# Kernel optimization log

Measured on AMD Instinct MI355X. Metric: run time of the kernel, lower is better.

Reference implementation:

```python
import jax, jax.numpy as jnp
import numpy as np

B, T, C, H = 2, 2048, 1024, 16
HS = C // H            # head_size = 64
HID = 2730             # 2*((2*(4*C)//3 + 1)//2) with multiple_of=2
EPS = 1e-6


def setup_inputs() -> dict:
    key = jax.random.key(0)
    ks = jax.random.split(key, 10)
    s = 0.02
    x = jax.random.normal(ks[0], (B, T, C), dtype=jnp.float32)
    Wq = jax.random.normal(ks[1], (H, HS, C), dtype=jnp.float32) * s
    Wk = jax.random.normal(ks[2], (H, HS, C), dtype=jnp.float32) * s
    Wv = jax.random.normal(ks[3], (H, HS, C), dtype=jnp.float32) * s
    Wo = jax.random.normal(ks[4], (C, C), dtype=jnp.float32) * s
    bo = jnp.zeros((C,), jnp.float32)
    w1 = jax.random.normal(ks[5], (HID, C), dtype=jnp.float32) * s
    b1 = jnp.zeros((HID,), jnp.float32)
    w2 = jax.random.normal(ks[6], (HID, C), dtype=jnp.float32) * s
    b2 = jnp.zeros((HID,), jnp.float32)
    w3 = jax.random.normal(ks[7], (C, HID), dtype=jnp.float32) * s
    b3 = jnp.zeros((C,), jnp.float32)
    ln1_w = jnp.ones((C,), jnp.float32)
    ln2_w = jnp.ones((C,), jnp.float32)
    # RoPE tables: freqs_cis = polar(1, outer(t, 1/theta^(2i/d)))
    inv = 1.0 / (10000.0 ** (jnp.arange(0, HS, 2, dtype=jnp.float32) / HS))  # [HS/2]
    ang = jnp.arange(T, dtype=jnp.float32)[:, None] * inv[None, :]           # [T, HS/2]
    return dict(x=x, ln1_w=ln1_w, Wq=Wq, Wk=Wk, Wv=Wv, Wo=Wo, bo=bo,
                w1=w1, b1=b1, w2=w2, b2=b2, w3=w3, b3=b3, ln2_w=ln2_w,
                cos=jnp.cos(ang), sin=jnp.sin(ang))


def _rmsnorm(x, w):
    return x / jnp.sqrt(jnp.mean(x * x, axis=-1, keepdims=True) + EPS) * w


def _rope(x, cos, sin):
    # x: [B,H,T,HS]; cos/sin: [T, HS/2] -> complex rotation on (even,odd) pairs
    xr = x.reshape(*x.shape[:-1], HS // 2, 2)
    x0, x1 = xr[..., 0], xr[..., 1]
    c = cos[None, None]; s = sin[None, None]
    o0 = x0 * c - x1 * s
    o1 = x0 * s + x1 * c
    return jnp.stack([o0, o1], axis=-1).reshape(x.shape)


def _swish_bug(x):
    # faithful to source: x * (1/1 + exp(-x)) == x * (1 + exp(-x))
    return x * (1.0 + jnp.exp(-x))


def reference(x, ln1_w, Wq, Wk, Wv, Wo, bo, w1, b1, w2, b2, w3, b3, ln2_w, cos, sin):
    # Block (norm='rms'): x = l1(x); x = x + attn(x); x = l2(x); x = x + ffn(x)
    x1 = _rmsnorm(x, ln1_w)
    # batched per-head projections (Linear has no bias in Head)
    q = jnp.einsum('btc,hdc->bhtd', x1, Wq)
    k = jnp.einsum('btc,hdc->bhtd', x1, Wk)
    v = jnp.einsum('btc,hdc->bhtd', x1, Wv)
    # source: xq,xk = apply_rotary_emb(key, query); query,key = xq,xk;
    # wei = key @ query^T == rot(query) @ rot(key)^T  -> standard attention
    q = _rope(q, cos, sin)
    k = _rope(k, cos, sin)
    scores = jnp.einsum('bhtd,bhsd->bhts', q, k) * (HS ** -0.5)
    mask = jnp.tril(jnp.ones((T, T), dtype=bool))
    scores = jnp.where(mask[None, None], scores, -jnp.inf)
    wei = jax.nn.softmax(scores, axis=-1)
    attn = jnp.einsum('bhts,bhsd->bhtd', wei, v)
    attn = attn.transpose(0, 2, 1, 3).reshape(B, T, C)  # concat heads
    attn = attn @ Wo.T + bo
    x2 = x1 + attn
    x3 = _rmsnorm(x2, ln2_w)
    h = _swish_bug(x3 @ w1.T + b1) * (x3 @ w2.T + b2)
    ffn = h @ w3.T + b3
    return x3 + ffn
```

## Files before the change

kernel.cpp:

```cpp
#include <hip/hip_runtime.h>
#include <hip/hip_bf16.h>

#define Bv 2
#define Tv 2048
#define Cv 1024
#define Hv 16
#define HSv 64
#define HIDv 2730
#define HIDP 2816
#define Mv 4096

using bf16x8 = __attribute__((ext_vector_type(8))) __bf16;
using f32x4  = __attribute__((ext_vector_type(4))) float;
typedef unsigned long long ull;

__device__ __forceinline__ void gload_lds16(const void* g, void* l) {
    auto gp = (const __attribute__((address_space(1))) unsigned int*)(unsigned long long)(uintptr_t)g;
    auto lp = (__attribute__((address_space(3))) unsigned int*)(unsigned int)(uintptr_t)l;
    __builtin_amdgcn_global_load_lds(gp, lp, 16, 0, 0);
}

struct CastSeg { const float* s; __bf16* d; long nsrc; long ntot; int sc; int dc; };
struct CastArgs { CastSeg seg[7]; };

__global__ __launch_bounds__(256) void k_castall(CastArgs a) {
    long gid = (long)blockIdx.x * 256 + threadIdx.x;
    long gstr = (long)gridDim.x * 256;
#pragma unroll 1
    for (int g = 0; g < 7; ++g) {
        CastSeg sg = a.seg[g];
        if (sg.sc == 0) {
            long n4 = sg.ntot >> 2;
            for (long i = gid; i < n4; i += gstr) {
                long base = i * 4;
                float4 v = {0.f, 0.f, 0.f, 0.f};
                if (base < sg.nsrc) v = *(const float4*)(sg.s + base);
                __bf16 o[4] = {(__bf16)v.x, (__bf16)v.y, (__bf16)v.z, (__bf16)v.w};
                *(ull*)(sg.d + base) = *(ull*)o;
            }
        } else {
            long n8 = sg.ntot >> 3;
            for (long i8 = gid; i8 < n8; i8 += gstr) {
                long base = i8 * 8;
                int r = (int)(base / sg.dc), c = (int)(base % sg.dc);
                __bf16 o[8];
                const float* srow = sg.s + (long)r * sg.sc + c;
                if (c + 8 <= sg.sc) {
#pragma unroll
                    for (int q = 0; q < 4; ++q) {
                        float2 v = *(const float2*)(srow + q * 2);
                        o[q * 2] = (__bf16)v.x; o[q * 2 + 1] = (__bf16)v.y;
                    }
                } else {
#pragma unroll
                    for (int e = 0; e < 8; ++e)
                        o[e] = (c + e < sg.sc) ? (__bf16)srow[e] : (__bf16)0.0f;
                }
                *(bf16x8*)(sg.d + base) = *(bf16x8*)o;
            }
        }
    }
}

__global__ __launch_bounds__(256) void k_rmsnorm(const float* __restrict__ x,
                                                 const float* __restrict__ w,
                                                 float* __restrict__ yf,
                                                 __bf16* __restrict__ yh) {
    int row = blockIdx.x;
    const float4* xr = (const float4*)(x + (size_t)row * Cv);
    float4 a = xr[threadIdx.x];
    float ss = a.x * a.x + a.y * a.y + a.z * a.z + a.w * a.w;
#pragma unroll
    for (int m = 1; m < 64; m <<= 1) ss += __shfl_xor(ss, m);
    __shared__ float red[4];
    if ((threadIdx.x & 63) == 0) red[threadIdx.x >> 6] = ss;
    __syncthreads();
    float tot = red[0] + red[1] + red[2] + red[3];
    float sc = rsqrtf(tot * (1.0f / Cv) + 1e-6f);
    float4 wv = ((const float4*)w)[threadIdx.x];
    float4 o;
    o.x = a.x * sc * wv.x; o.y = a.y * sc * wv.y;
    o.z = a.z * sc * wv.z; o.w = a.w * sc * wv.w;
    ((float4*)(yf + (size_t)row * Cv))[threadIdx.x] = o;
    __bf16* yp = yh + (size_t)row * Cv + threadIdx.x * 4;
    yp[0] = (__bf16)o.x; yp[1] = (__bf16)o.y; yp[2] = (__bf16)o.z; yp[3] = (__bf16)o.w;
}

template <int BM, int EPI>
__global__ __launch_bounds__(256) void k_gemm(
    const __bf16* __restrict__ A, const __bf16* __restrict__ Bm,
    int M, int N, int K,
    float* __restrict__ outF,
    const float* __restrict__ bias,
    const float* __restrict__ resid,
    __bf16* __restrict__ qOut, __bf16* __restrict__ kOut, __bf16* __restrict__ vOut,
    const float* __restrict__ cosT, const float* __restrict__ sinT) {
    constexpr int NN = (BM == 128) ? 4 : 2;
    __shared__ __align__(16) __bf16 As[BM][64];
    __shared__ __align__(16) __bf16 Bs[128][64];
    int tid = threadIdx.x, lane = tid & 63, wave = tid >> 6;
    int nm = M / BM;
    int nwg = nm * (N >> 7);
    int flat = blockIdx.x;
    int orig = (flat & 7) * (nwg >> 3) + (flat >> 3);
    int m0 = (orig % nm) * BM;
    int n0 = (orig / nm) * 128;
    int wro = (BM == 128) ? (wave >> 1) * 64 : 0;
    int wco = (BM == 128) ? (wave & 1) * 64 : wave * 32;
    int fr = lane & 15, fo2 = (lane >> 4) * 16;
    int lr = lane >> 3, lc = (lane & 7) * 8;
    f32x4 acc[4][NN] = {};
    for (int k0 = 0; k0 < K; k0 += 64) {
        __syncthreads();
        int arow0 = wave * (BM / 4);
#pragma unroll
        for (int i = 0; i < BM / 32; ++i) {
            int r = arow0 + i * 8 + lr;
            gload_lds16(A + (long)(m0 + r) * K + k0 + (lc ^ ((r & 7) << 3)), &As[r][lc]);
        }
        int brow0 = wave * 32;
#pragma unroll
        for (int i = 0; i < 4; ++i) {
            int r = brow0 + i * 8 + lr;
            gload_lds16(Bm + (long)(n0 + r) * K + k0 + (lc ^ ((r & 7) << 3)), &Bs[r][lc]);
        }
        __syncthreads();
#pragma unroll
        for (int s = 0; s < 2; ++s) {
            bf16x8 af[4], bf[NN];
#pragma unroll
            for (int m = 0; m < 4; ++m) {
                int r = wro + m * 16 + fr;
                af[m] = *(const bf16x8*)((const char*)&As[r][0] + ((s * 64 + fo2) ^ ((r & 7) << 4)));
            }
#pragma unroll
            for (int n = 0; n < NN; ++n) {
                int r = wco + n * 16 + fr;
                bf[n] = *(const bf16x8*)((const char*)&Bs[r][0] + ((s * 64 + fo2) ^ ((r & 7) << 4)));
            }
            __builtin_amdgcn_s_setprio(1);
#pragma unroll
            for (int m = 0; m < 4; ++m)
#pragma unroll
                for (int n = 0; n < NN; ++n)
                    acc[m][n] = __builtin_amdgcn_mfma_f32_16x16x32_bf16(af[m], bf[n], acc[m][n], 0, 0, 0);
            __builtin_amdgcn_s_setprio(0);
        }
    }
    int fq = (lane >> 4) * 4;
    if (EPI == 1) {
#pragma unroll
        for (int m = 0; m < 4; ++m)
#pragma unroll
            for (int n = 0; n < NN; ++n) {
                int row = m0 + wro + m * 16 + fq;
                int col = n0 + wco + n * 16 + fr;
#pragma unroll
                for (int r = 0; r < 4; ++r) {
                    float v = acc[m][n][r];
                    long idx = (long)(row + r) * N + col;
                    if (bias) v += bias[col];
                    if (resid) v += resid[idx];
                    outF[idx] = v;
                }
            }
    } else {
        const float SCL = 0.125f * 1.44269504f;
#pragma unroll
        for (int n = 0; n < NN; ++n) {
            int col = n0 + wco + n * 16 + fr;
            int part = col >> 10;
            int cn = col & 1023;
            int hh = cn >> 6, d = cn & 63, ii = d >> 1;
            bool evn = (d & 1) == 0;
#pragma unroll
            for (int m = 0; m < 4; ++m) {
                int row = m0 + wro + m * 16 + fq;
                int bh = (row >> 11) * 16 + hh;
                int tb = row & (Tv - 1);
                if (part == 2) {
                    int X = (d & 7) << 3;
                    int tile0 = tb & ~63, toff = tb & 63;
                    __bf16 ov[4];
#pragma unroll
                    for (int r = 0; r < 4; ++r) ov[r] = (__bf16)acc[m][n][r];
                    *(ull*)(vOut + ((long)bh * 64 + d) * Tv + tile0 + (toff ^ X)) = *(ull*)ov;
                } else {
                    float pxv[4];
#pragma unroll
                    for (int r = 0; r < 4; ++r) pxv[r] = __shfl_xor(acc[m][n][r], 1);
                    if (evn) {
#pragma unroll
                        for (int r = 0; r < 4; ++r) {
                            int t = tb + r;
                            float c = cosT[t * 32 + ii], s = sinT[t * 32 + ii];
                            float x0 = acc[m][n][r], x1 = pxv[r];
                            float r0 = x0 * c - x1 * s;
                            float r1 = x0 * s + x1 * c;
                            if (part == 0) {
                                __bf16 pr[2] = {(__bf16)(r0 * SCL), (__bf16)(r1 * SCL)};
                                *(unsigned int*)(qOut + (long)(row + r) * 1024 + cn) = *(unsigned int*)pr;
                            } else {
                                __bf16 pr[2] = {(__bf16)r0, (__bf16)r1};
                                char* base = (char*)(kOut + ((long)bh * Tv + t) * 64);
                                *(unsigned int*)(base + ((4 * ii) ^ ((t & 7) << 4))) = *(unsigned int*)pr;
                            }
                        }
                    }
                }
            }
        }
    }
}

__global__ __launch_bounds__(256, 2) void k_ffn(const __bf16* __restrict__ A,
                                                const __bf16* __restrict__ B1,
                                                const __bf16* __restrict__ B2,
                                                const float* __restrict__ b1,
                                                const float* __restrict__ b2,
                                                __bf16* __restrict__ outH) {
    __shared__ __align__(16) __bf16 As[128][64];
    __shared__ __align__(16) __bf16 B1s[128][64];
    __shared__ __align__(16) __bf16 B2s[128][64];
    int tid = threadIdx.x, lane = tid & 63, wave = tid >> 6;
    int nwg = 32 * (HIDP >> 7);
    int flat = blockIdx.x;
    int orig = (flat & 7) * (nwg >> 3) + (flat >> 3);
    int m0 = (orig & 31) * 128;
    int n0 = (orig >> 5) * 128;
    int wro = (wave >> 1) * 64, wco = (wave & 1) * 64;
    int fr = lane & 15, fo2 = (lane >> 4) * 16;
    int sr = tid >> 3, sc = (tid & 7) * 8;
    f32x4 acc1[4][4] = {}, acc2[4][4] = {};
    for (int k0 = 0; k0 < Cv; k0 += 64) {
        __syncthreads();
#pragma unroll
        for (int i = 0; i < 4; ++i) {
            int r = i * 32 + sr;
            int scs = sc ^ ((r & 7) << 3);
            gload_lds16(A  + (long)(m0 + r) * Cv + k0 + scs, &As[r][sc]);
            gload_lds16(B1 + (long)(n0 + r) * Cv + k0 + scs, &B1s[r][sc]);
            gload_lds16(B2 + (long)(n0 + r) * Cv + k0 + scs, &B2s[r][sc]);
        }
        __syncthreads();
#pragma unroll
        for (int s = 0; s < 2; ++s) {
            bf16x8 af[4], b1f[4], b2f[4];
#pragma unroll
            for (int m = 0; m < 4; ++m) {
                int r = wro + m * 16 + fr;
                af[m] = *(const bf16x8*)((const char*)&As[r][0] + ((s * 64 + fo2) ^ ((r & 7) << 4)));
            }
#pragma unroll
            for (int n = 0; n < 4; ++n) {
                int r = wco + n * 16 + fr;
                b1f[n] = *(const bf16x8*)((const char*)&B1s[r][0] + ((s * 64 + fo2) ^ ((r & 7) << 4)));
                b2f[n] = *(const bf16x8*)((const char*)&B2s[r][0] + ((s * 64 + fo2) ^ ((r & 7) << 4)));
            }
            __builtin_amdgcn_s_setprio(1);
#pragma unroll
            for (int m = 0; m < 4; ++m)
#pragma unroll
                for (int n = 0; n < 4; ++n) {
                    acc1[m][n] = __builtin_amdgcn_mfma_f32_16x16x32_bf16(af[m], b1f[n], acc1[m][n], 0, 0, 0);
                    acc2[m][n] = __builtin_amdgcn_mfma_f32_16x16x32_bf16(af[m], b2f[n], acc2[m][n], 0, 0, 0);
                }
            __builtin_amdgcn_s_setprio(0);
        }
    }
    int fq = (lane >> 4) * 4;
#pragma unroll
    for (int m = 0; m < 4; ++m)
#pragma unroll
        for (int n = 0; n < 4; ++n) {
            int row = m0 + wro + m * 16 + fq;
            int col = n0 + wco + n * 16 + fr;
            float b1v = (col < HIDv) ? b1[col] : 0.0f;
            float b2v = (col < HIDv) ? b2[col] : 0.0f;
#pragma unroll
            for (int r = 0; r < 4; ++r) {
                float c1 = acc1[m][n][r] + b1v;
                float c2 = acc2[m][n][r] + b2v;
                float sw = c1 * (1.0f + __expf(-c1));
                outH[(long)(row + r) * HIDP + col] = (__bf16)(sw * c2);
            }
        }
}

__global__ __launch_bounds__(256) void k_attn(const __bf16* __restrict__ Q,
                                              const __bf16* __restrict__ KR,
                                              const __bf16* __restrict__ VT,
                                              __bf16* __restrict__ O) {
    __shared__ __align__(16) __bf16 Ks[2][128][64];
    __shared__ __align__(16) __bf16 Vs[2][64][128];
    __shared__ __align__(16) __bf16 Ps[4][2][16][64];
    int tid = threadIdx.x, lane = tid & 63, w = tid >> 6;
    int bh = blockIdx.x & 31;
    int qt = 15 - (blockIdx.x >> 5);
    int q0 = qt * 128;
    int b = bh >> 4, h = bh & 15;
    const long qbase = ((long)b * Tv) * Cv + h * HSv;
    const long kbase = (long)bh * Tv * 64;
    const long vbase = (long)bh * 64 * Tv;
    int fr = lane & 15, g = lane >> 4;
    int go = g * 8;
    int xr = (fr & 7) << 4;
    int qrowA = q0 + w * 16 + fr;
    int qrowB = q0 + 64 + w * 16 + fr;
    bf16x8 qA0 = *(const bf16x8*)(Q + qbase + (long)qrowA * Cv + go);
    bf16x8 qA1 = *(const bf16x8*)(Q + qbase + (long)qrowA * Cv + 32 + go);
    bf16x8 qB0 = *(const bf16x8*)(Q + qbase + (long)qrowB * Cv + go);
    bf16x8 qB1 = *(const bf16x8*)(Q + qbase + (long)qrowB * Cv + 32 + go);

    bf16x8 ones;
#pragma unroll
    for (int e = 0; e < 8; ++e) ones[e] = (__bf16)1.0f;

    f32x4 oA[4] = {}, oB[4] = {};
    f32x4 lsA = {}, lsB = {};
    float mA = -INFINITY, mB = -INFINITY;

    auto stage = [&](int j0, int bufi) {
#pragma unroll
        for (int i = 0; i < 4; ++i) {
            int rk = i * 32 + w * 8 + (lane >> 3);
            gload_lds16(KR + kbase + (long)(j0 + rk) * 64 + (lane & 7) * 8,
                        &Ks[bufi][rk][(lane & 7) * 8]);
        }
#pragma unroll
        for (int i = 0; i < 4; ++i) {
            int rv = w * 16 + i * 4 + (lane >> 4);
            gload_lds16(VT + vbase + (long)rv * Tv + j0 + (lane & 15) * 8,
                        &Vs[bufi][rv][(lane & 15) * 8]);
        }
    };

    stage(0, 0);
    for (int t = 0; t <= qt; ++t) {
        int cur = t & 1;
        __syncthreads();
        if (t < qt) stage((t + 1) * 128, cur ^ 1);
        bool diag = (t == qt);
        f32x4 sA[8], sB[8];
        __builtin_amdgcn_s_setprio(1);
#pragma unroll
        for (int kk = 0; kk < 8; ++kk) {
            int key = kk * 16 + fr;
            const char* krow = (const char*)&Ks[cur][key][0];
            bf16x8 kf0 = *(const bf16x8*)(krow + ((go * 2) ^ ((key & 7) << 4)));
            bf16x8 kf1 = *(const bf16x8*)(krow + ((64 + go * 2) ^ ((key & 7) << 4)));
            f32x4 zB = {};
            zB = __builtin_amdgcn_mfma_f32_16x16x32_bf16(kf0, qB0, zB, 0, 0, 0);
            zB = __builtin_amdgcn_mfma_f32_16x16x32_bf16(kf1, qB1, zB, 0, 0, 0);
            sB[kk] = zB;
            if (!(diag && kk >= 4)) {
                f32x4 zA = {};
                zA = __builtin_amdgcn_mfma_f32_16x16x32_bf16(kf0, qA0, zA, 0, 0, 0);
                zA = __builtin_amdgcn_mfma_f32_16x16x32_bf16(kf1, qA1, zA, 0, 0, 0);
                sA[kk] = zA;
            } else {
                f32x4 ninf = {-INFINITY, -INFINITY, -INFINITY, -INFINITY};
                sA[kk] = ninf;
            }
        }
        __builtin_amdgcn_s_setprio(0);
        if (diag) {
            int qlA = w * 16 + fr;
            int qlB = 64 + w * 16 + fr;
#pragma unroll
            for (int kk = 0; kk < 4; ++kk)
#pragma unroll
                for (int r = 0; r < 4; ++r) {
                    int key = kk * 16 + g * 4 + r;
                    if (key > qlA) sA[kk][r] = -INFINITY;
                }
#pragma unroll
            for (int kk = 4; kk < 8; ++kk)
#pragma unroll
                for (int r = 0; r < 4; ++r) {
                    int key = kk * 16 + g * 4 + r;
                    if (key > qlB) sB[kk][r] = -INFINITY;
                }
        }
        float pmA = sA[0][0], pmB = sB[0][0];
#pragma unroll
        for (int kk = 0; kk < 8; ++kk)
#pragma unroll
            for (int r = 0; r < 4; ++r) {
                pmA = fmaxf(pmA, sA[kk][r]);
                pmB = fmaxf(pmB, sB[kk][r]);
            }
        pmA = fmaxf(pmA, __shfl_xor(pmA, 16));
        pmA = fmaxf(pmA, __shfl_xor(pmA, 32));
        pmB = fmaxf(pmB, __shfl_xor(pmB, 16));
        pmB = fmaxf(pmB, __shfl_xor(pmB, 32));
        if (!__all(pmA - mA <= 8.0f)) {
            float mn = fmaxf(mA, pmA);
            float alpha = exp2f(mA - mn);
            mA = mn;
#pragma unroll
            for (int r = 0; r < 4; ++r) lsA[r] *= alpha;
#pragma unroll
            for (int fb = 0; fb < 4; ++fb)
#pragma unroll
                for (int r = 0; r < 4; ++r) oA[fb][r] *= alpha;
        }
        if (!__all(pmB - mB <= 8.0f)) {
            float mn = fmaxf(mB, pmB);
            float alpha = exp2f(mB - mn);
            mB = mn;
#pragma unroll
            for (int r = 0; r < 4; ++r) lsB[r] *= alpha;
#pragma unroll
            for (int fb = 0; fb < 4; ++fb)
#pragma unroll
                for (int r = 0; r < 4; ++r) oB[fb][r] *= alpha;
        }
        char* prA = (char*)&Ps[w][0][fr][0];
        char* prB = (char*)&Ps[w][1][fr][0];
#pragma unroll
        for (int hf = 0; hf < 2; ++hf) {
            bool actA = !(diag && hf == 1);
            if (actA) {
#pragma unroll
                for (int kk = 0; kk < 4; ++kk) {
                    int ks = hf * 4 + kk;
                    __bf16 pk[4];
#pragma unroll
                    for (int r = 0; r < 4; ++r) pk[r] = (__bf16)exp2f(sA[ks][r] - mA);
                    *(ull*)(prA + ((kk * 32 + g * 8) ^ xr)) = *(ull*)pk;
                }
            }
#pragma unroll
            for (int kk = 0; kk < 4; ++kk) {
                int ks = hf * 4 + kk;
                __bf16 pk[4];
#pragma unroll
                for (int r = 0; r < 4; ++r) pk[r] = (__bf16)exp2f(sB[ks][r] - mB);
                *(ull*)(prB + ((kk * 32 + g * 8) ^ xr)) = *(ull*)pk;
            }
            bf16x8 paA0, paA1;
            if (actA) {
                paA0 = *(const bf16x8*)(prA + ((g * 16) ^ xr));
                paA1 = *(const bf16x8*)(prA + ((64 + g * 16) ^ xr));
            }
            bf16x8 paB0 = *(const bf16x8*)(prB + ((g * 16) ^ xr));
            bf16x8 paB1 = *(const bf16x8*)(prB + ((64 + g * 16) ^ xr));
            __builtin_amdgcn_s_setprio(1);
            if (actA) {
                lsA = __builtin_amdgcn_mfma_f32_16x16x32_bf16(ones, paA0, lsA, 0, 0, 0);
                lsA = __builtin_amdgcn_mfma_f32_16x16x32_bf16(ones, paA1, lsA, 0, 0, 0);
            }
            lsB = __builtin_amdgcn_mfma_f32_16x16x32_bf16(ones, paB0, lsB, 0, 0, 0);
            lsB = __builtin_amdgcn_mfma_f32_16x16x32_bf16(ones, paB1, lsB, 0, 0, 0);
#pragma unroll
            for (int fb = 0; fb < 4; ++fb) {
                int vrow = fb * 16 + fr;
                const char* vrd = (const char*)&Vs[cur][vrow][0];
                bf16x8 v0 = *(const bf16x8*)(vrd + hf * 128 + ((go * 2) ^ ((vrow & 7) << 4)));
                bf16x8 v1 = *(const bf16x8*)(vrd + hf * 128 + ((64 + go * 2) ^ ((vrow & 7) << 4)));
                oB[fb] = __builtin_amdgcn_mfma_f32_16x16x32_bf16(v0, paB0, oB[fb], 0, 0, 0);
                oB[fb] = __builtin_amdgcn_mfma_f32_16x16x32_bf16(v1, paB1, oB[fb], 0, 0, 0);
                if (actA) {
                    oA[fb] = __builtin_amdgcn_mfma_f32_16x16x32_bf16(v0, paA0, oA[fb], 0, 0, 0);
                    oA[fb] = __builtin_amdgcn_mfma_f32_16x16x32_bf16(v1, paA1, oA[fb], 0, 0, 0);
                }
            }
            __builtin_amdgcn_s_setprio(0);
        }
    }
    float rlA = 1.0f / lsA[0], rlB = 1.0f / lsB[0];
#pragma unroll
    for (int fb = 0; fb < 4; ++fb) {
        __bf16 ovA[4], ovB[4];
#pragma unroll
        for (int r = 0; r < 4; ++r) {
            ovA[r] = (__bf16)(oA[fb][r] * rlA);
            ovB[r] = (__bf16)(oB[fb][r] * rlB);
        }
        *(ull*)(O + qbase + (long)qrowA * Cv + fb * 16 + g * 4) = *(ull*)ovA;
        *(ull*)(O + qbase + (long)qrowB * Cv + fb * 16 + g * 4) = *(ull*)ovB;
    }
}

extern "C" void kernel_launch(void* const* d_in, const int* in_sizes, int n_in,
                              void* d_out, int out_size, void* d_ws, size_t ws_size,
                              hipStream_t stream) {
    const float* x    = (const float*)d_in[0];
    const float* ln1w = (const float*)d_in[1];
    const float* Wq   = (const float*)d_in[2];
    const float* Wk   = (const float*)d_in[3];
    const float* Wv   = (const float*)d_in[4];
    const float* Wo   = (const float*)d_in[5];
    const float* bo   = (const float*)d_in[6];
    const float* w1   = (const float*)d_in[7];
    const float* b1   = (const float*)d_in[8];
    const float* w2   = (const float*)d_in[9];
    const float* b2   = (const float*)d_in[10];
    const float* w3   = (const float*)d_in[11];
    const float* b3   = (const float*)d_in[12];
    const float* ln2w = (const float*)d_in[13];
    const float* cosT = (const float*)d_in[14];
    const float* sinT = (const float*)d_in[15];
    float* out = (float*)d_out;

    char* p = (char*)d_ws;
    auto alloc = [&](size_t bytes) {
        char* r = p;
        p += (bytes + 255) & ~(size_t)255;
        return r;
    };
    float*  x1f = (float*)alloc((size_t)Mv * Cv * 4);
    __bf16* qh  = (__bf16*)alloc((size_t)Mv * Cv * 2);
    __bf16* ah  = (__bf16*)alloc((size_t)Mv * Cv * 2);
    float*  x3f = (float*)alloc((size_t)Mv * Cv * 4);
    __bf16* x1h = (__bf16*)alloc((size_t)Mv * Cv * 2);
    __bf16* x3h = (__bf16*)alloc((size_t)Mv * Cv * 2);
    __bf16* KR  = (__bf16*)alloc((size_t)Bv * Hv * Tv * HSv * 2);
    __bf16* VT  = (__bf16*)alloc((size_t)Bv * Hv * HSv * Tv * 2);
    __bf16* hh  = (__bf16*)alloc((size_t)Mv * HIDP * 2);
    __bf16* wqkvh = (__bf16*)alloc((size_t)3072 * Cv * 2);
    __bf16* woh = (__bf16*)alloc((size_t)Cv * Cv * 2);
    __bf16* w1h = (__bf16*)alloc((size_t)HIDP * Cv * 2);
    __bf16* w2h = (__bf16*)alloc((size_t)HIDP * Cv * 2);
    __bf16* w3h = (__bf16*)alloc((size_t)Cv * HIDP * 2);

    const long nCC = (long)Cv * Cv;
    CastArgs ca;
    ca.seg[0] = {Wq, wqkvh,           nCC, nCC, 0, 0};
    ca.seg[1] = {Wk, wqkvh + nCC,     nCC, nCC, 0, 0};
    ca.seg[2] = {Wv, wqkvh + 2 * nCC, nCC, nCC, 0, 0};
    ca.seg[3] = {Wo, woh,             nCC, nCC, 0, 0};
    ca.seg[4] = {w1, w1h, (long)HIDv * Cv, (long)HIDP * Cv, 0, 0};
    ca.seg[5] = {w2, w2h, (long)HIDv * Cv, (long)HIDP * Cv, 0, 0};
    ca.seg[6] = {w3, w3h, (long)Cv * HIDv, (long)Cv * HIDP, HIDv, HIDP};
    k_castall<<<2048, 256, 0, stream>>>(ca);

    k_rmsnorm<<<Mv, 256, 0, stream>>>(x, ln1w, x1f, x1h);

    k_gemm<128, 4><<<768, 256, 0, stream>>>(x1h, wqkvh, Mv, 3072, Cv,
        nullptr, nullptr, nullptr, qh, KR, VT, cosT, sinT);

    k_attn<<<512, 256, 0, stream>>>(qh, KR, VT, ah);

    k_gemm<64, 1><<<512, 256, 0, stream>>>(ah, woh, Mv, Cv, Cv,
        x1f, bo, x1f, nullptr, nullptr, nullptr, nullptr, nullptr);

    k_rmsnorm<<<Mv, 256, 0, stream>>>(x1f, ln2w, x3f, x3h);

    k_ffn<<<704, 256, 0, stream>>>(x3h, w1h, w2h, b1, b2, hh);

    k_gemm<64, 1><<<512, 256, 0, stream>>>(hh, w3h, Mv, Cv, HIDP,
        out, b3, x3f, nullptr, nullptr, nullptr, nullptr, nullptr);
}
```

Measured before the change: 272.2 us.

## Double-buffer LDS tiles in GEMM and FFN kernels to overlap loads with MFMA

Both the generic GEMM and the fused FFN GEMM now keep two LDS buffers per operand. At the top of each K step the kernel issues global-to-LDS loads for the next tile, then runs the MFMA work on the current tile, leaving one barrier per iteration instead of two. The aim is to hide global memory latency behind matrix math. The cost is doubled LDS use: the FFN kernel grows to about 96KB of LDS, so its launch bound drops to one block per CU, which lowers occupancy.

After: 298.2 us. 1.1x slower.

```diff
diff --git a/kernel.cpp b/kernel.cpp
--- a/kernel.cpp
+++ b/kernel.cpp
@@ -96,8 +96,8 @@
     __bf16* __restrict__ qOut, __bf16* __restrict__ kOut, __bf16* __restrict__ vOut,
     const float* __restrict__ cosT, const float* __restrict__ sinT) {
     constexpr int NN = (BM == 128) ? 4 : 2;
-    __shared__ __align__(16) __bf16 As[BM][64];
-    __shared__ __align__(16) __bf16 Bs[128][64];
+    __shared__ __align__(16) __bf16 As[2][BM][64];
+    __shared__ __align__(16) __bf16 Bs[2][128][64];
     int tid = threadIdx.x, lane = tid & 63, wave = tid >> 6;
     int nm = M / BM;
     int nwg = nm * (N >> 7);
@@ -110,33 +110,40 @@
     int fr = lane & 15, fo2 = (lane >> 4) * 16;
     int lr = lane >> 3, lc = (lane & 7) * 8;
     f32x4 acc[4][NN] = {};
-    for (int k0 = 0; k0 < K; k0 += 64) {
-        __syncthreads();
+
+    auto stageG = [&](int k0, int buf) {
         int arow0 = wave * (BM / 4);
 #pragma unroll
         for (int i = 0; i < BM / 32; ++i) {
             int r = arow0 + i * 8 + lr;
-            gload_lds16(A + (long)(m0 + r) * K + k0 + (lc ^ ((r & 7) << 3)), &As[r][lc]);
+            gload_lds16(A + (long)(m0 + r) * K + k0 + (lc ^ ((r & 7) << 3)), &As[buf][r][lc]);
         }
         int brow0 = wave * 32;
 #pragma unroll
         for (int i = 0; i < 4; ++i) {
             int r = brow0 + i * 8 + lr;
-            gload_lds16(Bm + (long)(n0 + r) * K + k0 + (lc ^ ((r & 7) << 3)), &Bs[r][lc]);
-        }
+            gload_lds16(Bm + (long)(n0 + r) * K + k0 + (lc ^ ((r & 7) << 3)), &Bs[buf][r][lc]);
+        }
+    };
+
+    int nt = K >> 6;
+    stageG(0, 0);
+    for (int t = 0; t < nt; ++t) {
+        int bc = t & 1;
         __syncthreads();
+        if (t + 1 < nt) stageG((t + 1) << 6, bc ^ 1);
 #pragma unroll
         for (int s = 0; s < 2; ++s) {
             bf16x8 af[4], bf[NN];
 #pragma unroll
             for (int m = 0; m < 4; ++m) {
                 int r = wro + m * 16 + fr;
-                af[m] = *(const bf16x8*)((const char*)&As[r][0] + ((s * 64 + fo2) ^ ((r & 7) << 4)));
+                af[m] = *(const bf16x8*)((const char*)&As[bc][r][0] + ((s * 64 + fo2) ^ ((r & 7) << 4)));
             }
 #pragma unroll
             for (int n = 0; n < NN; ++n) {
                 int r = wco + n * 16 + fr;
-                bf[n] = *(const bf16x8*)((const char*)&Bs[r][0] + ((s * 64 + fo2) ^ ((r & 7) << 4)));
+                bf[n] = *(const bf16x8*)((const char*)&Bs[bc][r][0] + ((s * 64 + fo2) ^ ((r & 7) << 4)));
             }
             __builtin_amdgcn_s_setprio(1);
 #pragma unroll
@@ -213,15 +220,15 @@
     }
 }
 
-__global__ __launch_bounds__(256, 2) void k_ffn(const __bf16* __restrict__ A,
+__global__ __launch_bounds__(256, 1) void k_ffn(const __bf16* __restrict__ A,
                                                 const __bf16* __restrict__ B1,
                                                 const __bf16* __restrict__ B2,
                                                 const float* __restrict__ b1,
                                                 const float* __restrict__ b2,
                                                 __bf16* __restrict__ outH) {
-    __shared__ __align__(16) __bf16 As[128][64];
-    __shared__ __align__(16) __bf16 B1s[128][64];
-    __shared__ __align__(16) __bf16 B2s[128][64];
+    __shared__ __align__(16) __bf16 As[2][128][64];
+    __shared__ __align__(16) __bf16 B1s[2][128][64];
+    __shared__ __align__(16) __bf16 B2s[2][128][64];
     int tid = threadIdx.x, lane = tid & 63, wave = tid >> 6;
     int nwg = 32 * (HIDP >> 7);
     int flat = blockIdx.x;
@@ -232,30 +239,36 @@
     int fr = lane & 15, fo2 = (lane >> 4) * 16;
     int sr = tid >> 3, sc = (tid & 7) * 8;
     f32x4 acc1[4][4] = {}, acc2[4][4] = {};
-    for (int k0 = 0; k0 < Cv; k0 += 64) {
-        __syncthreads();
+
+    auto stageF = [&](int k0, int buf) {
 #pragma unroll
         for (int i = 0; i < 4; ++i) {
             int r = i * 32 + sr;
             int scs = sc ^ ((r & 7) << 3);
-            gload_lds16(A  + (long)(m0 + r) * Cv + k0 + scs, &As[r][sc]);
-            gload_lds16(B1 + (long)(n0 + r) * Cv + k0 + scs, &B1s[r][sc]);
-            gload_lds16(B2 + (long)(n0 + r) * Cv + k0 + scs, &B2s[r][sc]);
-        }
+            gload_lds16(A  + (long)(m0 + r) * Cv + k0 + scs, &As[buf][r][sc]);
+            gload_lds16(B1 + (long)(n0 + r) * Cv + k0 + scs, &B1s[buf][r][sc]);
+            gload_lds16(B2 + (long)(n0 + r) * Cv + k0 + scs, &B2s[buf][r][sc]);
+        }
+    };
+
+    stageF(0, 0);
+    for (int t = 0; t < Cv / 64; ++t) {
+        int bc = t & 1;
         __syncthreads();
+        if (t + 1 < Cv / 64) stageF((t + 1) << 6, bc ^ 1);
 #pragma unroll
         for (int s = 0; s < 2; ++s) {
             bf16x8 af[4], b1f[4], b2f[4];
 #pragma unroll
             for (int m = 0; m < 4; ++m) {
                 int r = wro + m * 16 + fr;
-                af[m] = *(const bf16x8*)((const char*)&As[r][0] + ((s * 64 + fo2) ^ ((r & 7) << 4)));
+                af[m] = *(const bf16x8*)((const char*)&As[bc][r][0] + ((s * 64 + fo2) ^ ((r & 7) << 4)));
             }
 #pragma unroll
             for (int n = 0; n < 4; ++n) {
                 int r = wco + n * 16 + fr;
-                b1f[n] = *(const bf16x8*)((const char*)&B1s[r][0] + ((s * 64 + fo2) ^ ((r & 7) << 4)));
-                b2f[n] = *(const bf16x8*)((const char*)&B2s[r][0] + ((s * 64 + fo2) ^ ((r & 7) << 4)));
+                b1f[n] = *(const bf16x8*)((const char*)&B1s[bc][r][0] + ((s * 64 + fo2) ^ ((r & 7) << 4)));
+                b2f[n] = *(const bf16x8*)((const char*)&B2s[bc][r][0] + ((s * 64 + fo2) ^ ((r & 7) << 4)));
             }
             __builtin_amdgcn_s_setprio(1);
 #pragma unroll
```

## Split attention into 64-row query tiles with single-buffered K/V staging

Applied to the files above, without the earlier changes.

The attention kernel now gives each block 64 query rows, one 16-row fragment per wave, instead of 128 rows. This doubles the grid to 1024 blocks and halves the per-wave accumulator and register state. K/V tiles are single-buffered, so the next tile loads only after a barrier at the end of each iteration. Diagonal-tile work is trimmed per wave. The aim is more occupancy and better load balance across the causal triangle, at the cost of losing load/compute overlap and reloading each K/V tile for twice as many blocks.

New measurement: 261.1 us. -4.1%, faster.

```diff
diff --git a/kernel.cpp b/kernel.cpp
--- a/kernel.cpp
+++ b/kernel.cpp
@@ -291,13 +291,14 @@
                                               const __bf16* __restrict__ KR,
                                               const __bf16* __restrict__ VT,
                                               __bf16* __restrict__ O) {
-    __shared__ __align__(16) __bf16 Ks[2][128][64];
-    __shared__ __align__(16) __bf16 Vs[2][64][128];
-    __shared__ __align__(16) __bf16 Ps[4][2][16][64];
+    __shared__ __align__(16) __bf16 Ks[128][64];
+    __shared__ __align__(16) __bf16 Vs[64][128];
+    __shared__ __align__(16) __bf16 Ps[4][16][64];
     int tid = threadIdx.x, lane = tid & 63, w = tid >> 6;
     int bh = blockIdx.x & 31;
-    int qt = 15 - (blockIdx.x >> 5);
-    int q0 = qt * 128;
+    int qt = 31 - (blockIdx.x >> 5);
+    int q0 = qt * 64;
+    int hi = qt & 1;
     int b = bh >> 4, h = bh & 15;
     const long qbase = ((long)b * Tv) * Cv + h * HSv;
     const long kbase = (long)bh * Tv * 64;
@@ -305,181 +306,126 @@
     int fr = lane & 15, g = lane >> 4;
     int go = g * 8;
     int xr = (fr & 7) << 4;
-    int qrowA = q0 + w * 16 + fr;
-    int qrowB = q0 + 64 + w * 16 + fr;
-    bf16x8 qA0 = *(const bf16x8*)(Q + qbase + (long)qrowA * Cv + go);
-    bf16x8 qA1 = *(const bf16x8*)(Q + qbase + (long)qrowA * Cv + 32 + go);
-    bf16x8 qB0 = *(const bf16x8*)(Q + qbase + (long)qrowB * Cv + go);
-    bf16x8 qB1 = *(const bf16x8*)(Q + qbase + (long)qrowB * Cv + 32 + go);
+    int qrow = q0 + w * 16 + fr;
+    bf16x8 qf0 = *(const bf16x8*)(Q + qbase + (long)qrow * Cv + go);
+    bf16x8 qf1 = *(const bf16x8*)(Q + qbase + (long)qrow * Cv + 32 + go);
 
     bf16x8 ones;
 #pragma unroll
     for (int e = 0; e < 8; ++e) ones[e] = (__bf16)1.0f;
 
-    f32x4 oA[4] = {}, oB[4] = {};
-    f32x4 lsA = {}, lsB = {};
-    float mA = -INFINITY, mB = -INFINITY;
-
-    auto stage = [&](int j0, int bufi) {
+    f32x4 o[4] = {};
+    f32x4 ls = {};
+    float mrow = -INFINITY;
+
+    auto stage = [&](int j0) {
 #pragma unroll
         for (int i = 0; i < 4; ++i) {
             int rk = i * 32 + w * 8 + (lane >> 3);
             gload_lds16(KR + kbase + (long)(j0 + rk) * 64 + (lane & 7) * 8,
-                        &Ks[bufi][rk][(lane & 7) * 8]);
+                        &Ks[rk][(lane & 7) * 8]);
         }
 #pragma unroll
         for (int i = 0; i < 4; ++i) {
             int rv = w * 16 + i * 4 + (lane >> 4);
             gload_lds16(VT + vbase + (long)rv * Tv + j0 + (lane & 15) * 8,
-                        &Vs[bufi][rv][(lane & 15) * 8]);
+                        &Vs[rv][(lane & 15) * 8]);
         }
     };
 
-    stage(0, 0);
-    for (int t = 0; t <= qt; ++t) {
-        int cur = t & 1;
+    int nt = (qt >> 1) + 1;
+    stage(0);
+    for (int t = 0; t < nt; ++t) {
         __syncthreads();
-        if (t < qt) stage((t + 1) * 128, cur ^ 1);
-        bool diag = (t == qt);
-        f32x4 sA[8], sB[8];
+        bool diag = (t == nt - 1);
+        int kkmax = diag ? (w + (hi ? 4 : 0)) : 7;
+        f32x4 s4[8];
         __builtin_amdgcn_s_setprio(1);
 #pragma unroll
         for (int kk = 0; kk < 8; ++kk) {
-            int key = kk * 16 + fr;
-            const char* krow = (const char*)&Ks[cur][key][0];
-            bf16x8 kf0 = *(const bf16x8*)(krow + ((go * 2) ^ ((key & 7) << 4)));
-            bf16x8 kf1 = *(const bf16x8*)(krow + ((64 + go * 2) ^ ((key & 7) << 4)));
-            f32x4 zB = {};
-            zB = __builtin_amdgcn_mfma_f32_16x16x32_bf16(kf0, qB0, zB, 0, 0, 0);
-            zB = __builtin_amdgcn_mfma_f32_16x16x32_bf16(kf1, qB1, zB, 0, 0, 0);
-            sB[kk] = zB;
-            if (!(diag && kk >= 4)) {
-                f32x4 zA = {};
-                zA = __builtin_amdgcn_mfma_f32_16x16x32_bf16(kf0, qA0, zA, 0, 0, 0);
-                zA = __builtin_amdgcn_mfma_f32_16x16x32_bf16(kf1, qA1, zA, 0, 0, 0);
-                sA[kk] = zA;
+            if (kk <= kkmax) {
+                int key = kk * 16 + fr;
+                const char* krow = (const char*)&Ks[key][0];
+                bf16x8 kf0 = *(const bf16x8*)(krow + ((go * 2) ^ ((key & 7) << 4)));
+                bf16x8 kf1 = *(const bf16x8*)(krow + ((64 + go * 2) ^ ((key & 7) << 4)));
+                f32x4 z = {};
+                z = __builtin_amdgcn_mfma_f32_16x16x32_bf16(kf0, qf0, z, 0, 0, 0);
+                z = __builtin_amdgcn_mfma_f32_16x16x32_bf16(kf1, qf1, z, 0, 0, 0);
+                s4[kk] = z;
             } else {
                 f32x4 ninf = {-INFINITY, -INFINITY, -INFINITY, -INFINITY};
-                sA[kk] = ninf;
+                s4[kk] = ninf;
             }
         }
         __builtin_amdgcn_s_setprio(0);
         if (diag) {
-            int qlA = w * 16 + fr;
-            int qlB = 64 + w * 16 + fr;
-#pragma unroll
-            for (int kk = 0; kk < 4; ++kk)
+            int qloc = hi * 64 + w * 16 + fr;
+#pragma unroll
+            for (int kk = 0; kk < 8; ++kk)
 #pragma unroll
                 for (int r = 0; r < 4; ++r) {
                     int key = kk * 16 + g * 4 + r;
-                    if (key > qlA) sA[kk][r] = -INFINITY;
+                    if (key > qloc) s4[kk][r] = -INFINITY;
                 }
-#pragma unroll
-            for (int kk = 4; kk < 8; ++kk)
-#pragma unroll
-                for (int r = 0; r < 4; ++r) {
-                    int key = kk * 16 + g * 4 + r;
-                    if (key > qlB) sB[kk][r] = -INFINITY;
-                }
-        }
-        float pmA = sA[0][0], pmB = sB[0][0];
+        }
+        float pmax = s4[0][0];
 #pragma unroll
         for (int kk = 0; kk < 8; ++kk)
 #pragma unroll
-            for (int r = 0; r < 4; ++r) {
-                pmA = fmaxf(pmA, sA[kk][r]);
-                pmB = fmaxf(pmB, sB[kk][r]);
-            }
-        pmA = fmaxf(pmA, __shfl_xor(pmA, 16));
-        pmA = fmaxf(pmA, __shfl_xor(pmA, 32));
-        pmB = fmaxf(pmB, __shfl_xor(pmB, 16));
-        pmB = fmaxf(pmB, __shfl_xor(pmB, 32));
-        if (!__all(pmA - mA <= 8.0f)) {
-            float mn = fmaxf(mA, pmA);
-            float alpha = exp2f(mA - mn);
-            mA = mn;
-#pragma unroll
-            for (int r = 0; r < 4; ++r) lsA[r] *= alpha;
+            for (int r = 0; r < 4; ++r) pmax = fmaxf(pmax, s4[kk][r]);
+        pmax = fmaxf(pmax, __shfl_xor(pmax, 16));
+        pmax = fmaxf(pmax, __shfl_xor(pmax, 32));
+        if (!__all(pmax - mrow <= 8.0f)) {
+            float mn = fmaxf(mrow, pmax);
+            float alpha = exp2f(mrow - mn);
+            mrow = mn;
+#pragma unroll
+            for (int r = 0; r < 4; ++r) ls[r] *= alpha;
 #pragma unroll
             for (int fb = 0; fb < 4; ++fb)
 #pragma unroll
-                for (int r = 0; r < 4; ++r) oA[fb][r] *= alpha;
-        }
-        if (!__all(pmB - mB <= 8.0f)) {
-            float mn = fmaxf(mB, pmB);
-            float alpha = exp2f(mB - mn);
-            mB = mn;
-#pragma unroll
-            for (int r = 0; r < 4; ++r) lsB[r] *= alpha;
-#pragma unroll
-            for (int fb = 0; fb < 4; ++fb)
-#pragma unroll
-                for (int r = 0; r < 4; ++r) oB[fb][r] *= alpha;
-        }
-        char* prA = (char*)&Ps[w][0][fr][0];
-        char* prB = (char*)&Ps[w][1][fr][0];
+                for (int r = 0; r < 4; ++r) o[fb][r] *= alpha;
+        }
+        char* prow = (char*)&Ps[w][fr][0];
 #pragma unroll
         for (int hf = 0; hf < 2; ++hf) {
-            bool actA = !(diag && hf == 1);
-            if (actA) {
-#pragma unroll
-                for (int kk = 0; kk < 4; ++kk) {
-                    int ks = hf * 4 + kk;
-                    __bf16 pk[4];
-#pragma unroll
-                    for (int r = 0; r < 4; ++r) pk[r] = (__bf16)exp2f(sA[ks][r] - mA);
-                    *(ull*)(prA + ((kk * 32 + g * 8) ^ xr)) = *(ull*)pk;
-                }
-            }
+            if (diag && !hi && hf == 1) break;
 #pragma unroll
             for (int kk = 0; kk < 4; ++kk) {
                 int ks = hf * 4 + kk;
                 __bf16 pk[4];
 #pragma unroll
-                for (int r = 0; r < 4; ++r) pk[r] = (__bf16)exp2f(sB[ks][r] - mB);
-                *(ull*)(prB + ((kk * 32 + g * 8) ^ xr)) = *(ull*)pk;
-            }
-            bf16x8 paA0, paA1;
-            if (actA) {
-                paA0 = *(const bf16x8*)(prA + ((g * 16) ^ xr));
-                paA1 = *(const bf16x8*)(prA + ((64 + g * 16) ^ xr));
-            }
-            bf16x8 paB0 = *(const bf16x8*)(prB + ((g * 16) ^ xr));
-            bf16x8 paB1 = *(const bf16x8*)(prB + ((64 + g * 16) ^ xr));
+                for (int r = 0; r < 4; ++r) pk[r] = (__bf16)exp2f(s4[ks][r] - mrow);
+                *(ull*)(prow + ((kk * 32 + g * 8) ^ xr)) = *(ull*)pk;
+            }
+            bf16x8 pa0 = *(const bf16x8*)(prow + ((g * 16) ^ xr));
+            bf16x8 pa1 = *(const bf16x8*)(prow + ((64 + g * 16) ^ xr));
             __builtin_amdgcn_s_setprio(1);
-            if (actA) {
-                lsA = __builtin_amdgcn_mfma_f32_16x16x32_bf16(ones, paA0, lsA, 0, 0, 0);
-                lsA = __builtin_amdgcn_mfma_f32_16x16x32_bf16(ones, paA1, lsA, 0, 0, 0);
-            }
-            lsB = __builtin_amdgcn_mfma_f32_16x16x32_bf16(ones, paB0, lsB, 0, 0, 0);
-            lsB = __builtin_amdgcn_mfma_f32_16x16x32_bf16(ones, paB1, lsB, 0, 0, 0);
+            ls = __builtin_amdgcn_mfma_f32_16x16x32_bf16(ones, pa0, ls, 0, 0, 0);
+            ls = __builtin_amdgcn_mfma_f32_16x16x32_bf16(ones, pa1, ls, 0, 0, 0);
 #pragma unroll
             for (int fb = 0; fb < 4; ++fb) {
                 int vrow = fb * 16 + fr;
-                const char* vrd = (const char*)&Vs[cur][vrow][0];
+                const char* vrd = (const char*)&Vs[vrow][0];
                 bf16x8 v0 = *(const bf16x8*)(vrd + hf * 128 + ((go * 2) ^ ((vrow & 7) << 4)));
                 bf16x8 v1 = *(const bf16x8*)(vrd + hf * 128 + ((64 + go * 2) ^ ((vrow & 7) << 4)));
-                oB[fb] = __builtin_amdgcn_mfma_f32_16x16x32_bf16(v0, paB0, oB[fb], 0, 0, 0);
-                oB[fb] = __builtin_amdgcn_mfma_f32_16x16x32_bf16(v1, paB1, oB[fb], 0, 0, 0);
-                if (actA) {
-                    oA[fb] = __builtin_amdgcn_mfma_f32_16x16x32_bf16(v0, paA0, oA[fb], 0, 0, 0);
-                    oA[fb] = __builtin_amdgcn_mfma_f32_16x16x32_bf16(v1, paA1, oA[fb], 0, 0, 0);
-                }
+                o[fb] = __builtin_amdgcn_mfma_f32_16x16x32_bf16(v0, pa0, o[fb], 0, 0, 0);
+                o[fb] = __builtin_amdgcn_mfma_f32_16x16x32_bf16(v1, pa1, o[fb], 0, 0, 0);
             }
             __builtin_amdgcn_s_setprio(0);
         }
+        if (t + 1 < nt) {
+            __syncthreads();
+            stage((t + 1) * 128);
+        }
     }
-    float rlA = 1.0f / lsA[0], rlB = 1.0f / lsB[0];
+    float rl = 1.0f / ls[0];
 #pragma unroll
     for (int fb = 0; fb < 4; ++fb) {
-        __bf16 ovA[4], ovB[4];
-#pragma unroll
-        for (int r = 0; r < 4; ++r) {
-            ovA[r] = (__bf16)(oA[fb][r] * rlA);
-            ovB[r] = (__bf16)(oB[fb][r] * rlB);
-        }
-        *(ull*)(O + qbase + (long)qrowA * Cv + fb * 16 + g * 4) = *(ull*)ovA;
-        *(ull*)(O + qbase + (long)qrowB * Cv + fb * 16 + g * 4) = *(ull*)ovB;
+        __bf16 ov[4];
+#pragma unroll
+        for (int r = 0; r < 4; ++r) ov[r] = (__bf16)(o[fb][r] * rl);
+        *(ull*)(O + qbase + (long)qrow * Cv + fb * 16 + g * 4) = *(ull*)ov;
     }
 }
 
@@ -541,7 +487,7 @@
     k_gemm<128, 4><<<768, 256, 0, stream>>>(x1h, wqkvh, Mv, 3072, Cv,
         nullptr, nullptr, nullptr, qh, KR, VT, cosT, sinT);
 
-    k_attn<<<512, 256, 0, stream>>>(qh, KR, VT, ah);
+    k_attn<<<1024, 256, 0, stream>>>(qh, KR, VT, ah);
 
     k_gemm<64, 1><<<512, 256, 0, stream>>>(ah, woh, Mv, Cv, Cv,
         x1f, bo, x1f, nullptr, nullptr, nullptr, nullptr, nullptr);
```
